# Kernel optimization log

Measured on AMD Instinct MI355X. Metric: run time of the kernel, lower is better.

The kernel has to match this reference:

```python
import jax, jax.numpy as jnp
import numpy as np

ATT_DIM = 64

def setup_inputs() -> dict:
    key = jax.random.key(0)
    kq, kk, kv = jax.random.split(key, 3)
    B, S, D = 4, 4096, ATT_DIM
    Q = jax.random.normal(kq, (B, S, D), dtype=jnp.float32)
    K = jax.random.normal(kk, (B, S, D), dtype=jnp.float32)
    V = jax.random.normal(kv, (B, S, D), dtype=jnp.float32)
    return {"Q": Q, "K": K, "V": V}

def reference(Q, K, V):
    # scores: [B, Sq, Sk]
    scale = 1.0 / jnp.sqrt(jnp.asarray(ATT_DIM, Q.dtype))
    scores = jnp.einsum('bqd,bkd->bqk', Q, K) * scale
    probs = jax.nn.softmax(scores, axis=-1)
    return jnp.einsum('bqk,bkd->bqd', probs, V)
```

## Files before the change

kernel.cpp:

```cpp
#include <hip/hip_runtime.h>


#define BATCH 4
#define SEQ   4096
#define DIM   64
#define KVB   32
#define NQ    16384
#define QSCALE 0.18033688011112042f

typedef float f32x16 __attribute__((ext_vector_type(16)));
typedef unsigned short u16x8 __attribute__((ext_vector_type(8)));
typedef unsigned int   u32x4 __attribute__((ext_vector_type(4)));
typedef unsigned int   u32x2 __attribute__((ext_vector_type(2)));

#define MFMA32(a, b, c) __builtin_amdgcn_mfma_f32_32x32x16_bf16((a), (b), (c), 0, 0, 0)
#define EXP2F(x) __builtin_amdgcn_exp2f(x)

__device__ __forceinline__ void plswap(unsigned int& a, unsigned int& b) {
  u32x2 r = __builtin_amdgcn_permlane32_swap(a, b, false, false);
  a = r[0]; b = r[1];
}
__device__ __forceinline__ void xswap32f(float x, float& a, float& b) {
  unsigned int u = __float_as_uint(x), v = u;
  plswap(u, v);
  a = __uint_as_float(u); b = __uint_as_float(v);
}

__device__ __forceinline__ unsigned short f2bf(float x) {
  unsigned int u = __float_as_uint(x);
  return (unsigned short)((u + 0x7fffu + ((u >> 16) & 1u)) >> 16);
}
__device__ __forceinline__ unsigned int cvtpk(float a, float b) {
  unsigned int r;
  asm("v_cvt_pk_bf16_f32 %0, %1, %2" : "=v"(r) : "v"(a), "v"(b));
  return r;
}

__global__ __launch_bounds__(256) void prep_kernel(
    const float* __restrict__ K, const float* __restrict__ V,
    unsigned short* __restrict__ Kf, unsigned short* __restrict__ Vf) {
  __shared__ float tk[64][65];
  __shared__ float tv[64][65];
  const int t = threadIdx.x;
  const int b = blockIdx.x >> 6;
  const int s0 = (blockIdx.x & 63) << 6;
  #pragma unroll
  for (int r = 0; r < 4; ++r) {
    const int s_loc = r * 16 + (t >> 4);
    const int d0 = (t & 15) << 2;
    const long base = ((long)b * SEQ + s0 + s_loc) * DIM + d0;
    const float4 kv = *(const float4*)(K + base);
    const float4 vv = *(const float4*)(V + base);
    tk[s_loc][d0 + 0] = kv.x; tk[s_loc][d0 + 1] = kv.y;
    tk[s_loc][d0 + 2] = kv.z; tk[s_loc][d0 + 3] = kv.w;
    tv[s_loc][d0 + 0] = vv.x; tv[s_loc][d0 + 1] = vv.y;
    tv[s_loc][d0 + 2] = vv.z; tv[s_loc][d0 + 3] = vv.w;
  }
  __syncthreads();
  const int l  = t >> 2;
  const int j0 = (t & 3) << 1;
  const int l5 = l & 31, b5 = l >> 5;
  #pragma unroll
  for (int kh = 0; kh < 2; ++kh) {
    #pragma unroll
    for (int ch = 0; ch < 4; ++ch) {
      const int key = kh * 32 + l5;
      const int d   = ch * 16 + b5 * 8 + j0;
      ushort2 w;
      w.x = f2bf(tk[key][d]);
      w.y = f2bf(tk[key][d + 1]);
      const long kb32 = (s0 >> 5) + kh;
      const long off = (((long)b * 128 + kb32) * 4 + ch) * 512 + 2 * t;
      *(ushort2*)(Kf + off) = w;
    }
  }
  #pragma unroll
  for (int dh = 0; dh < 2; ++dh) {
    #pragma unroll
    for (int ks = 0; ks < 4; ++ks) {
      const int key0 = ks * 16 + b5 * 8 + j0;
      const int d    = dh * 32 + l5;
      ushort2 w;
      w.x = f2bf(tv[key0][d]);
      w.y = f2bf(tv[key0 + 1][d]);
      const long kb64 = (s0 >> 6);
      const long off = ((((long)b * 64 + kb64) * 2 + dh) * 4 + ks) * 512 + 2 * t;
      *(ushort2*)(Vf + off) = w;
    }
  }
}

template<int NS>
__global__ __launch_bounds__(256, 4) void attn_kernel(
    const float* __restrict__ Q,
    const unsigned short* __restrict__ Kf, const unsigned short* __restrict__ Vf,
    float* __restrict__ Opart, float* __restrict__ Lpart) {

  __shared__ __align__(16) unsigned short tiles[2][8 * 512];

  constexpr int SPL = SEQ / NS;
  constexpr int NT  = SPL / KVB;
  constexpr int NWG = 4 * NS * 32;
  constexpr int CPX = NWG / 8;

  const int raw = blockIdx.x;
  const int bid = (raw & 7) * CPX + (raw >> 3);
  const int b     = bid / (NS * 32);
  const int rem   = bid % (NS * 32);
  const int split = rem >> 5;
  const int qblk  = rem & 31;

  const int tid  = threadIdx.x;
  const int wave = tid >> 6;
  const int lane = tid & 63;
  const int l5   = lane & 31;
  const int b5   = lane >> 5;

  const int qrow0 = qblk * 128 + wave * 32;
  const int kv0   = split * SPL;

  u16x8 qh[4];
  {
    const float* qp = Q + ((long)b * SEQ + qrow0 + l5) * DIM;
    #pragma unroll
    for (int ch = 0; ch < 4; ++ch) {
      const float* p = qp + ch * 16 + b5 * 8;
      float4 x0 = *(const float4*)(p);
      float4 x1 = *(const float4*)(p + 4);
      u32x4 qw = {cvtpk(x0.x * QSCALE, x0.y * QSCALE),
                  cvtpk(x0.z * QSCALE, x0.w * QSCALE),
                  cvtpk(x1.x * QSCALE, x1.y * QSCALE),
                  cvtpk(x1.z * QSCALE, x1.w * QSCALE)};
      qh[ch] = __builtin_bit_cast(u16x8, qw);
    }
  }

  auto stage = [&](int buf, int t) {
    const int kb32 = (kv0 >> 5) + t;
    #pragma unroll
    for (int i = 0; i < 2; ++i) {
      const unsigned short* src;
      int blk;
      if (wave < 2) {
        const int ch = wave * 2 + i;
        src = Kf + (((long)b * 128 + kb32) * 4 + ch) * 512 + lane * 8;
        blk = ch;
      } else {
        const int dh = wave - 2;
        const int kb64 = kb32 >> 1;
        const int ks = (t & 1) * 2 + i;
        src = Vf + ((((long)b * 64 + kb64) * 2 + dh) * 4 + ks) * 512 + lane * 8;
        blk = 4 + dh * 2 + i;
      }
      __builtin_amdgcn_global_load_lds(
          (__attribute__((address_space(1))) void*)src,
          (__attribute__((address_space(3))) void*)(&tiles[buf][blk * 512] + lane * 8),
          16, 0, 0);
    }
  };

  stage(0, 0);
  __syncthreads();

  f32x16 O0 = {0,0,0,0,0,0,0,0,0,0,0,0,0,0,0,0};
  f32x16 O1 = {0,0,0,0,0,0,0,0,0,0,0,0,0,0,0,0};
  float lsum = 0.0f;

  for (int t = 0; t < NT; ++t) {
    const int buf = t & 1;
    if (t + 1 < NT) stage(buf ^ 1, t + 1);

    const u16x8* fb = (const u16x8*)(&tiles[buf][0]) + lane;

    f32x16 sc = {0,0,0,0,0,0,0,0,0,0,0,0,0,0,0,0};
    __builtin_amdgcn_s_setprio(1);
    sc = MFMA32(fb[0 * 64], qh[0], sc);
    sc = MFMA32(fb[1 * 64], qh[1], sc);
    sc = MFMA32(fb[2 * 64], qh[2], sc);
    sc = MFMA32(fb[3 * 64], qh[3], sc);
    __builtin_amdgcn_s_setprio(0);

    float p[16];
    #pragma unroll
    for (int r = 0; r < 16; ++r) p[r] = EXP2F(sc[r]);
    {
      float u[8];
      #pragma unroll
      for (int r = 0; r < 8; ++r) u[r] = p[r] + p[r + 8];
      #pragma unroll
      for (int r = 0; r < 4; ++r) u[r] += u[r + 4];
      lsum += (u[0] + u[1]) + (u[2] + u[3]);
    }

    auto pack8 = [&](float a0, float a1, float a2, float a3,
                     float a4, float a5, float a6, float a7) -> u16x8 {
      unsigned int x0w = cvtpk(a0, a1), x1w = cvtpk(a2, a3);
      unsigned int y0w = cvtpk(a4, a5), y1w = cvtpk(a6, a7);
      plswap(x0w, y0w);
      plswap(x1w, y1w);
      u32x4 hw = {x0w, x1w, y0w, y1w};
      return __builtin_bit_cast(u16x8, hw);
    };
    u16x8 pb0 = pack8(p[0], p[1], p[2],  p[3],  p[4],  p[5],  p[6],  p[7]);
    u16x8 pb1 = pack8(p[8], p[9], p[10], p[11], p[12], p[13], p[14], p[15]);

    __builtin_amdgcn_s_setprio(1);
    O0 = MFMA32(fb[4 * 64], pb0, O0);  O1 = MFMA32(fb[6 * 64], pb0, O1);
    O0 = MFMA32(fb[5 * 64], pb1, O0);  O1 = MFMA32(fb[7 * 64], pb1, O1);
    __builtin_amdgcn_s_setprio(0);

    __syncthreads();
  }

  {
    float la, lb2;
    xswap32f(lsum, la, lb2);
    lsum = la + lb2;
  }

  float* ob = Opart + (long)split * (NQ * DIM)
            + ((long)((b * 32 + qblk) * 4 + wave) * 2) * 1024 + lane * 16;
  *(float4*)(ob +  0) = float4{O0[0],  O0[1],  O0[2],  O0[3]};
  *(float4*)(ob +  4) = float4{O0[4],  O0[5],  O0[6],  O0[7]};
  *(float4*)(ob +  8) = float4{O0[8],  O0[9],  O0[10], O0[11]};
  *(float4*)(ob + 12) = float4{O0[12], O0[13], O0[14], O0[15]};
  *(float4*)(ob + 1024 +  0) = float4{O1[0],  O1[1],  O1[2],  O1[3]};
  *(float4*)(ob + 1024 +  4) = float4{O1[4],  O1[5],  O1[6],  O1[7]};
  *(float4*)(ob + 1024 +  8) = float4{O1[8],  O1[9],  O1[10], O1[11]};
  *(float4*)(ob + 1024 + 12) = float4{O1[12], O1[13], O1[14], O1[15]};
  if (lane < 32) {
    long qg = (long)b * SEQ + qrow0 + lane;
    Lpart[(long)split * NQ + qg] = lsum;
  }
}

template<int NS>
__global__ __launch_bounds__(256) void merge_kernel(
    const float* __restrict__ Opart, const float* __restrict__ Lpart,
    float* __restrict__ Out) {
  int idx = blockIdx.x * 256 + threadIdx.x;
  int bq = idx >> 4;
  int d4 = (idx & 15) << 2;
  int b    = bq >> 12;
  int qrow = bq & 4095;
  int qblk = qrow >> 7;
  int wv   = (qrow >> 5) & 3;
  int l5   = qrow & 31;
  int mt   = d4 >> 5;
  int d5   = d4 & 31;
  int b5v  = (d5 >> 2) & 1;
  int g    = d5 >> 3;
  int lane = b5v * 32 + l5;
  long off = ((long)((b * 32 + qblk) * 4 + wv) * 2 + mt) * 1024 + lane * 16 + g * 4;

  float4 acc = {0, 0, 0, 0};
  float L = 0.0f;
  #pragma unroll
  for (int s = 0; s < NS; ++s) {
    float4 o = *(const float4*)(Opart + (long)s * (NQ * DIM) + off);
    acc.x += o.x; acc.y += o.y; acc.z += o.z; acc.w += o.w;
    L += Lpart[(long)s * NQ + bq];
  }
  float inv = 1.0f / L;
  *(float4*)(Out + (long)bq * DIM + d4) =
      float4{acc.x * inv, acc.y * inv, acc.z * inv, acc.w * inv};
}

extern "C" void kernel_launch(void* const* d_in, const int* in_sizes, int n_in,
                              void* d_out, int out_size, void* d_ws, size_t ws_size,
                              hipStream_t stream) {
  const float* Q = (const float*)d_in[0];
  const float* K = (const float*)d_in[1];
  const float* V = (const float*)d_in[2];
  float* Out = (float*)d_out;

  unsigned short* w16 = (unsigned short*)d_ws;
  unsigned short* Kf  = w16;
  unsigned short* Vf  = w16 + 1048576;
  float* wsf = (float*)(w16 + 2097152);

  const size_t need8 = (size_t)4 * 1024 * 1024 + (size_t)8 * NQ * DIM * 4
                     + (size_t)8 * NQ * 4;
  const int ns = (ws_size >= need8) ? 8 : 4;

  prep_kernel<<<dim3(256), dim3(256), 0, stream>>>(K, V, Kf, Vf);
  if (ns == 8) {
    float* Opart = wsf;
    float* Lpart = wsf + (size_t)8 * NQ * DIM;
    attn_kernel<8><<<dim3(1024), dim3(256), 0, stream>>>(Q, Kf, Vf, Opart, Lpart);
    merge_kernel<8><<<dim3(1024), dim3(256), 0, stream>>>(Opart, Lpart, Out);
  } else {
    float* Opart = wsf;
    float* Lpart = wsf + (size_t)4 * NQ * DIM;
    attn_kernel<4><<<dim3(512), dim3(256), 0, stream>>>(Q, Kf, Vf, Opart, Lpart);
    merge_kernel<4><<<dim3(1024), dim3(256), 0, stream>>>(Opart, Lpart, Out);
  }
}
```

Before: 48.59 us.

## Double KV tile to 64 keys per iteration with simplified contiguous staging

Raises the KV block from 32 to 64 keys per loop iteration and doubles the LDS double buffer. This halves the number of barriers and iterations and exposes two independent score MFMA chains for interleaving. The staging logic now uses contiguous 4-chunk loads per wave instead of per-wave index arithmetic. The cost is more LDS and register use per workgroup, which may reduce occupancy.

```diff
diff --git a/kernel.cpp b/kernel.cpp
--- a/kernel.cpp
+++ b/kernel.cpp
@@ -4,7 +4,7 @@
 #define BATCH 4
 #define SEQ   4096
 #define DIM   64
-#define KVB   32
+#define KVB   64
 #define NQ    16384
 #define QSCALE 0.18033688011112042f
 
@@ -96,7 +96,7 @@
     const unsigned short* __restrict__ Kf, const unsigned short* __restrict__ Vf,
     float* __restrict__ Opart, float* __restrict__ Lpart) {
 
-  __shared__ __align__(16) unsigned short tiles[2][8 * 512];
+  __shared__ __align__(16) unsigned short tiles[2][16 * 512];
 
   constexpr int SPL = SEQ / NS;
   constexpr int NT  = SPL / KVB;
@@ -135,28 +135,20 @@
     }
   }
 
+  const int kvrole = wave >> 1;
+  const int lb     = (wave & 1) * 4;
+  const unsigned short* gsrc =
+      kvrole ? Vf + (((long)b * 64 + (kv0 >> 6)) * 8) * 512
+             : Kf + (((long)b * 128 + (kv0 >> 5)) * 4) * 512;
+
   auto stage = [&](int buf, int t) {
-    const int kb32 = (kv0 >> 5) + t;
+    const unsigned short* s = gsrc + (long)t * 4096 + lb * 512 + lane * 8;
+    unsigned short* d = &tiles[buf][(kvrole * 8 + lb) * 512];
     #pragma unroll
-    for (int i = 0; i < 2; ++i) {
-      const unsigned short* src;
-      int blk;
-      if (wave < 2) {
-        const int ch = wave * 2 + i;
-        src = Kf + (((long)b * 128 + kb32) * 4 + ch) * 512 + lane * 8;
-        blk = ch;
-      } else {
-        const int dh = wave - 2;
-        const int kb64 = kb32 >> 1;
-        const int ks = (t & 1) * 2 + i;
-        src = Vf + ((((long)b * 64 + kb64) * 2 + dh) * 4 + ks) * 512 + lane * 8;
-        blk = 4 + dh * 2 + i;
-      }
+    for (int i = 0; i < 4; ++i)
       __builtin_amdgcn_global_load_lds(
-          (__attribute__((address_space(1))) void*)src,
-          (__attribute__((address_space(3))) void*)(&tiles[buf][blk * 512] + lane * 8),
-          16, 0, 0);
-    }
+          (__attribute__((address_space(1))) void*)(s + i * 512),
+          (__attribute__((address_space(3))) void*)(d + i * 512), 16, 0, 0);
   };
 
   stage(0, 0);
@@ -172,42 +164,70 @@
 
     const u16x8* fb = (const u16x8*)(&tiles[buf][0]) + lane;
 
-    f32x16 sc = {0,0,0,0,0,0,0,0,0,0,0,0,0,0,0,0};
+    f32x16 sc0 = {0,0,0,0,0,0,0,0,0,0,0,0,0,0,0,0};
+    f32x16 sc1 = {0,0,0,0,0,0,0,0,0,0,0,0,0,0,0,0};
     __builtin_amdgcn_s_setprio(1);
-    sc = MFMA32(fb[0 * 64], qh[0], sc);
-    sc = MFMA32(fb[1 * 64], qh[1], sc);
-    sc = MFMA32(fb[2 * 64], qh[2], sc);
-    sc = MFMA32(fb[3 * 64], qh[3], sc);
+    sc0 = MFMA32(fb[0 * 64], qh[0], sc0);  sc1 = MFMA32(fb[4 * 64], qh[0], sc1);
+    sc0 = MFMA32(fb[1 * 64], qh[1], sc0);  sc1 = MFMA32(fb[5 * 64], qh[1], sc1);
+    sc0 = MFMA32(fb[2 * 64], qh[2], sc0);  sc1 = MFMA32(fb[6 * 64], qh[2], sc1);
+    sc0 = MFMA32(fb[3 * 64], qh[3], sc0);  sc1 = MFMA32(fb[7 * 64], qh[3], sc1);
     __builtin_amdgcn_s_setprio(0);
 
-    float p[16];
-    #pragma unroll
-    for (int r = 0; r < 16; ++r) p[r] = EXP2F(sc[r]);
     {
+      float p[16];
+      #pragma unroll
+      for (int r = 0; r < 16; ++r) p[r] = EXP2F(sc0[r]);
       float u[8];
       #pragma unroll
       for (int r = 0; r < 8; ++r) u[r] = p[r] + p[r + 8];
       #pragma unroll
       for (int r = 0; r < 4; ++r) u[r] += u[r + 4];
       lsum += (u[0] + u[1]) + (u[2] + u[3]);
-    }
-
-    auto pack8 = [&](float a0, float a1, float a2, float a3,
-                     float a4, float a5, float a6, float a7) -> u16x8 {
-      unsigned int x0w = cvtpk(a0, a1), x1w = cvtpk(a2, a3);
-      unsigned int y0w = cvtpk(a4, a5), y1w = cvtpk(a6, a7);
-      plswap(x0w, y0w);
-      plswap(x1w, y1w);
-      u32x4 hw = {x0w, x1w, y0w, y1w};
-      return __builtin_bit_cast(u16x8, hw);
-    };
-    u16x8 pb0 = pack8(p[0], p[1], p[2],  p[3],  p[4],  p[5],  p[6],  p[7]);
-    u16x8 pb1 = pack8(p[8], p[9], p[10], p[11], p[12], p[13], p[14], p[15]);
-
-    __builtin_amdgcn_s_setprio(1);
-    O0 = MFMA32(fb[4 * 64], pb0, O0);  O1 = MFMA32(fb[6 * 64], pb0, O1);
-    O0 = MFMA32(fb[5 * 64], pb1, O0);  O1 = MFMA32(fb[7 * 64], pb1, O1);
-    __builtin_amdgcn_s_setprio(0);
+
+      unsigned int a0 = cvtpk(p[0], p[1]),   a1 = cvtpk(p[2], p[3]);
+      unsigned int a2 = cvtpk(p[4], p[5]),   a3 = cvtpk(p[6], p[7]);
+      unsigned int c0 = cvtpk(p[8], p[9]),   c1 = cvtpk(p[10], p[11]);
+      unsigned int c2 = cvtpk(p[12], p[13]), c3 = cvtpk(p[14], p[15]);
+      plswap(a0, a2); plswap(a1, a3);
+      plswap(c0, c2); plswap(c1, c3);
+      u32x4 w0 = {a0, a1, a2, a3};
+      u32x4 w1 = {c0, c1, c2, c3};
+      u16x8 pb0 = __builtin_bit_cast(u16x8, w0);
+      u16x8 pb1 = __builtin_bit_cast(u16x8, w1);
+
+      __builtin_amdgcn_s_setprio(1);
+      O0 = MFMA32(fb[ 8 * 64], pb0, O0);  O1 = MFMA32(fb[12 * 64], pb0, O1);
+      O0 = MFMA32(fb[ 9 * 64], pb1, O0);  O1 = MFMA32(fb[13 * 64], pb1, O1);
+      __builtin_amdgcn_s_setprio(0);
+    }
+
+    {
+      float p[16];
+      #pragma unroll
+      for (int r = 0; r < 16; ++r) p[r] = EXP2F(sc1[r]);
+      float u[8];
+      #pragma unroll
+      for (int r = 0; r < 8; ++r) u[r] = p[r] + p[r + 8];
+      #pragma unroll
+      for (int r = 0; r < 4; ++r) u[r] += u[r + 4];
+      lsum += (u[0] + u[1]) + (u[2] + u[3]);
+
+      unsigned int a0 = cvtpk(p[0], p[1]),   a1 = cvtpk(p[2], p[3]);
+      unsigned int a2 = cvtpk(p[4], p[5]),   a3 = cvtpk(p[6], p[7]);
+      unsigned int c0 = cvtpk(p[8], p[9]),   c1 = cvtpk(p[10], p[11]);
+      unsigned int c2 = cvtpk(p[12], p[13]), c3 = cvtpk(p[14], p[15]);
+      plswap(a0, a2); plswap(a1, a3);
+      plswap(c0, c2); plswap(c1, c3);
+      u32x4 w0 = {a0, a1, a2, a3};
+      u32x4 w1 = {c0, c1, c2, c3};
+      u16x8 pb2 = __builtin_bit_cast(u16x8, w0);
+      u16x8 pb3 = __builtin_bit_cast(u16x8, w1);
+
+      __builtin_amdgcn_s_setprio(1);
+      O0 = MFMA32(fb[10 * 64], pb2, O0);  O1 = MFMA32(fb[14 * 64], pb2, O1);
+      O0 = MFMA32(fb[11 * 64], pb3, O0);  O1 = MFMA32(fb[15 * 64], pb3, O1);
+      __builtin_amdgcn_s_setprio(0);
+    }
 
     __syncthreads();
   }
```

Result: faster. 44.74 us (-7.9%).
